# Optimization experiments

Measured on AMD Instinct MI355X. Metric: run time of the kernel, lower is better.

The kernel has to match this reference:

```python
import jax, jax.numpy as jnp
import numpy as np

N_NODES = 100000
N_EDGES = 1600000
IN_DIM = 256
OUT_DIM = 64
LEAKY_SLOPE = 0.01  # torch F.leaky_relu default


def setup_inputs() -> dict:
    key = jax.random.key(0)
    k1, k2, k3, k4, k5 = jax.random.split(key, 5)
    h = jax.random.normal(k1, (N_NODES, IN_DIM), dtype=jnp.float32)
    W_fc = jax.random.normal(k2, (IN_DIM, OUT_DIM), dtype=jnp.float32) * (1.0 / np.sqrt(IN_DIM))
    a_attn = jax.random.normal(k3, (2 * OUT_DIM,), dtype=jnp.float32) * (1.0 / np.sqrt(2 * OUT_DIM))
    edge_src = jax.random.randint(k4, (N_EDGES,), 0, N_NODES, dtype=jnp.int32)
    edge_dst = jax.random.randint(k5, (N_EDGES,), 0, N_NODES, dtype=jnp.int32)
    return {"h": h, "W_fc": W_fc, "a_attn": a_attn, "edge_src": edge_src, "edge_dst": edge_dst}


def reference(h, W_fc, a_attn, edge_src, edge_dst):
    # z = fc(h)  (no bias)
    z = h @ W_fc                                   # [N, D]
    # edge attention: leaky_relu(concat(z_src, z_dst) @ a)
    # split a into src/dst halves -> node-level projections (same math, no concat)
    el = z @ a_attn[:OUT_DIM]                      # [N]
    er = z @ a_attn[OUT_DIM:]                      # [N]
    e = jax.nn.leaky_relu(el[edge_src] + er[edge_dst], negative_slope=LEAKY_SLOPE)  # [E]
    # segment softmax over destination-node mailboxes
    m = jax.ops.segment_max(e, edge_dst, num_segments=N_NODES)   # [N]
    ex = jnp.exp(e - m[edge_dst])                                # [E]
    s = jax.ops.segment_sum(ex, edge_dst, num_segments=N_NODES)  # [N]
    alpha = ex / s[edge_dst]                                     # [E]
    # weighted scatter-sum of neighbor features
    h_out = jax.ops.segment_sum(alpha[:, None] * z[edge_src], edge_dst, num_segments=N_NODES)  # [N, D]
    # heads != 1 branch: ELU (dropout = 0 in eval)
    return jax.nn.elu(h_out)
```

## Files before the change

### kernel.cpp

```cpp
#include <hip/hip_runtime.h>
#include <hip/hip_bf16.h>

#define IN_DIM 256
#define OUT_DIM 64
#define CHUNK 4096
#define BSH 8
#define P2CAP 6144

typedef short bf16x8 __attribute__((ext_vector_type(8)));
typedef float f32x4 __attribute__((ext_vector_type(4)));

__device__ inline unsigned short f2bf(float x) {
  unsigned int u = __float_as_uint(x);
  return (unsigned short)((u + 0x7FFFu + ((u >> 16) & 1u)) >> 16);
}

__global__ __launch_bounds__(256) void k_prep(const float* __restrict__ W,
                                              unsigned short* __restrict__ Wbf) {
  int f = blockIdx.x * 256 + threadIdx.x;
  int kc = f >> 8, ct = (f >> 6) & 3, q = (f >> 4) & 3, nq = f & 15;
  int col = ct * 16 + nq, k0 = kc * 32 + q * 8;
  unsigned short v[8];
#pragma unroll
  for (int j = 0; j < 8; ++j) v[j] = f2bf(W[(size_t)(k0 + j) * OUT_DIM + col]);
  *(uint4*)(Wbf + (size_t)f * 8) = *(uint4*)v;
}

__global__ __launch_bounds__(256) void k_gemm(const float* __restrict__ h,
                                              const unsigned short* __restrict__ Wbf,
                                              const float* __restrict__ a,
                                              unsigned short* __restrict__ zb,
                                              float* __restrict__ el,
                                              float* __restrict__ er, int n) {
  __shared__ unsigned short Ab[64][264];
  const int t = threadIdx.x;
  const int base = blockIdx.x * 64;

#pragma unroll
  for (int i = 0; i < 16; ++i) {
    int f = i * 256 + t;
    int r = f >> 6, c4 = f & 63;
    int row = base + r;
    float4 v = make_float4(0.f, 0.f, 0.f, 0.f);
    if (row < n) v = *(const float4*)(h + (size_t)row * IN_DIM + c4 * 4);
    unsigned int p0 = (unsigned int)f2bf(v.x) | ((unsigned int)f2bf(v.y) << 16);
    unsigned int p1 = (unsigned int)f2bf(v.z) | ((unsigned int)f2bf(v.w) << 16);
    *(uint2*)&Ab[r][c4 * 4] = make_uint2(p0, p1);
  }
  __syncthreads();

  const int w = t >> 6, lane = t & 63, nq = lane & 15, q = lane >> 4;

  f32x4 acc[4];
#pragma unroll
  for (int ct = 0; ct < 4; ++ct) acc[ct] = (f32x4){0.f, 0.f, 0.f, 0.f};

#pragma unroll
  for (int kc = 0; kc < 8; ++kc) {
    bf16x8 af = *(const bf16x8*)&Ab[w * 16 + nq][kc * 32 + q * 8];
#pragma unroll
    for (int ct = 0; ct < 4; ++ct) {
      bf16x8 bfr = *(const bf16x8*)(Wbf + (size_t)((kc * 4 + ct) * 64 + lane) * 8);
      acc[ct] = __builtin_amdgcn_mfma_f32_16x16x32_bf16(af, bfr, acc[ct], 0, 0, 0);
    }
  }

  float a1[4], a2[4];
#pragma unroll
  for (int ct = 0; ct < 4; ++ct) {
    a1[ct] = a[ct * 16 + nq];
    a2[ct] = a[OUT_DIM + ct * 16 + nq];
  }
#pragma unroll
  for (int r = 0; r < 4; ++r) {
    int orow = base + w * 16 + q * 4 + r;
    float p1 = 0.f, p2 = 0.f;
#pragma unroll
    for (int ct = 0; ct < 4; ++ct) {
      float v = acc[ct][r];
      p1 += v * a1[ct];
      p2 += v * a2[ct];
      if (orow < n) zb[(size_t)orow * OUT_DIM + ct * 16 + nq] = f2bf(v);
    }
    p1 += __shfl_xor(p1, 1); p1 += __shfl_xor(p1, 2);
    p1 += __shfl_xor(p1, 4); p1 += __shfl_xor(p1, 8);
    p2 += __shfl_xor(p2, 1); p2 += __shfl_xor(p2, 2);
    p2 += __shfl_xor(p2, 4); p2 += __shfl_xor(p2, 8);
    if (orow < n && nq == 0) { el[orow] = p1; er[orow] = p2; }
  }
}

__global__ __launch_bounds__(256) void k_p1hist(const int* __restrict__ dst,
                                                int* __restrict__ gh, int E,
                                                int nbuck, int b1) {
  __shared__ int hist[512];
  int t = threadIdx.x, b = blockIdx.x;
  hist[t] = 0;
  hist[t + 256] = 0;
  __syncthreads();
  int beg = b * CHUNK;
#pragma unroll
  for (int i = t; i < CHUNK; i += 256) {
    int e = beg + i;
    if (e < E) atomicAdd(&hist[dst[e] >> BSH], 1);
  }
  __syncthreads();
  for (int i = t; i < nbuck; i += 256) gh[i * b1 + b] = hist[i];
}

__global__ __launch_bounds__(256) void k_scanA(const int* __restrict__ in,
                                               int* __restrict__ out,
                                               int* __restrict__ bsum, int N) {
  __shared__ int wtot[4];
  int t = threadIdx.x, lane = t & 63, w = t >> 6;
  int idx = blockIdx.x * 1024 + t * 4;
  int d0 = idx + 0 < N ? in[idx + 0] : 0;
  int d1 = idx + 1 < N ? in[idx + 1] : 0;
  int d2 = idx + 2 < N ? in[idx + 2] : 0;
  int d3 = idx + 3 < N ? in[idx + 3] : 0;
  int tsum = d0 + d1 + d2 + d3;
  int incl = tsum;
  for (int o = 1; o < 64; o <<= 1) {
    int v = __shfl_up(incl, o);
    if (lane >= o) incl += v;
  }
  if (lane == 63) wtot[w] = incl;
  __syncthreads();
  int woff = 0;
  for (int i = 0; i < 4; ++i)
    if (i < w) woff += wtot[i];
  int btot = wtot[0] + wtot[1] + wtot[2] + wtot[3];
  int e = woff + incl - tsum;
  if (idx + 0 < N) out[idx + 0] = e; e += d0;
  if (idx + 1 < N) out[idx + 1] = e; e += d1;
  if (idx + 2 < N) out[idx + 2] = e; e += d2;
  if (idx + 3 < N) out[idx + 3] = e;
  if (t == 0) bsum[blockIdx.x] = btot;
}

__global__ __launch_bounds__(256) void k_scanB(int* __restrict__ bsum, int nb) {
  __shared__ int wtot[4];
  int t = threadIdx.x, lane = t & 63, w = t >> 6;
  int v = t < nb ? bsum[t] : 0;
  int incl = v;
  for (int o = 1; o < 64; o <<= 1) {
    int u = __shfl_up(incl, o);
    if (lane >= o) incl += u;
  }
  if (lane == 63) wtot[w] = incl;
  __syncthreads();
  int woff = 0;
  for (int i = 0; i < 4; ++i)
    if (i < w) woff += wtot[i];
  if (t < nb) bsum[t] = woff + incl - v;
}

__global__ __launch_bounds__(256) void k_scanC2(int* __restrict__ out,
                                                const int* __restrict__ bsum, int M) {
  int i = blockIdx.x * 256 + threadIdx.x;
  if (i < M) out[i] += bsum[i >> 10];
}

__global__ __launch_bounds__(256) void k_p1scat(const int* __restrict__ src,
                                                const int* __restrict__ dst,
                                                const int* __restrict__ pbase,
                                                int2* __restrict__ pairs, int E,
                                                int nbuck, int b1) {
  __shared__ int pb[512];
  __shared__ int cur[512];
  int t = threadIdx.x, b = blockIdx.x;
  for (int i = t; i < 512; i += 256) {
    pb[i] = (i < nbuck) ? pbase[i * b1 + b] : 0;
    cur[i] = 0;
  }
  __syncthreads();
  int beg = b * CHUNK;
#pragma unroll
  for (int i = t; i < CHUNK; i += 256) {
    int e = beg + i;
    if (e < E) {
      int d = dst[e], s = src[e];
      int bk = d >> BSH;
      int r = atomicAdd(&cur[bk], 1);
      pairs[pb[bk] + r] = make_int2(d, s);
    }
  }
}

__global__ __launch_bounds__(256) void k_p2(const int2* __restrict__ pairs,
                                            const int* __restrict__ pbase,
                                            int* __restrict__ ssrc,
                                            int* __restrict__ off, int E, int n,
                                            int nbuck, int b1) {
  __shared__ int deg[256];
  __shared__ int loff[256];
  __shared__ int cur[256];
  __shared__ int stage[P2CAP];
  __shared__ int wtot[4];
  int t = threadIdx.x, b = blockIdx.x;
  int beg = pbase[b * b1];
  int end = (b + 1 < nbuck) ? pbase[(b + 1) * b1] : E;
  int cnt = end - beg;
  int base = b << BSH;
  deg[t] = 0;
  __syncthreads();
  for (int i = t; i < cnt; i += 256) atomicAdd(&deg[pairs[beg + i].x - base], 1);
  __syncthreads();
  int v = deg[t];
  int lane = t & 63, w = t >> 6;
  int inc = v;
  for (int o = 1; o < 64; o <<= 1) {
    int u = __shfl_up(inc, o);
    if (lane >= o) inc += u;
  }
  if (lane == 63) wtot[w] = inc;
  __syncthreads();
  int woff = 0;
  for (int i = 0; i < 4; ++i)
    if (i < w) woff += wtot[i];
  int ex = woff + inc - v;
  loff[t] = ex;
  cur[t] = ex;
  __syncthreads();
  for (int i = t; i < cnt; i += 256) {
    int2 p = pairs[beg + i];
    int r = atomicAdd(&cur[p.x - base], 1);
    if (r < P2CAP) stage[r] = p.y;
  }
  __syncthreads();
  for (int i = t; i < cnt; i += 256) ssrc[beg + i] = stage[i];
  int node = base + t;
  if (node <= n) off[node] = beg + loff[t];
}

__global__ __launch_bounds__(256) void k_agg(const int* __restrict__ off,
                                             const int* __restrict__ ssrc,
                                             const float* __restrict__ el,
                                             const float* __restrict__ er,
                                             const unsigned short* __restrict__ zb,
                                             float* __restrict__ out, int N) {
  int t = threadIdx.x;
  int node = blockIdx.x * 16 + (t >> 4);
  if (node >= N) return;
  int cq = (t & 15) * 4;
  int beg = off[node], end = off[node + 1];
  float erd = er[node];
  float ax = 0.f, ay = 0.f, az = 0.f, aw = 0.f, ssum = 0.f;
  int j = beg;
  for (; j + 4 <= end; j += 4) {
    int s0 = ssrc[j], s1 = ssrc[j + 1], s2 = ssrc[j + 2], s3 = ssrc[j + 3];
    uint2 z0 = *(const uint2*)(zb + (s0 << 6) + cq);
    uint2 z1 = *(const uint2*)(zb + (s1 << 6) + cq);
    uint2 z2 = *(const uint2*)(zb + (s2 << 6) + cq);
    uint2 z3 = *(const uint2*)(zb + (s3 << 6) + cq);
    float x0 = el[s0] + erd, x1 = el[s1] + erd;
    float x2 = el[s2] + erd, x3 = el[s3] + erd;
    x0 = x0 > 0.f ? x0 : 0.01f * x0;
    x1 = x1 > 0.f ? x1 : 0.01f * x1;
    x2 = x2 > 0.f ? x2 : 0.01f * x2;
    x3 = x3 > 0.f ? x3 : 0.01f * x3;
    float e0 = __expf(x0), e1 = __expf(x1), e2 = __expf(x2), e3 = __expf(x3);
    ssum += (e0 + e1) + (e2 + e3);
    ax += e0 * __uint_as_float(z0.x << 16) + e1 * __uint_as_float(z1.x << 16) +
          e2 * __uint_as_float(z2.x << 16) + e3 * __uint_as_float(z3.x << 16);
    ay += e0 * __uint_as_float(z0.x & 0xFFFF0000u) + e1 * __uint_as_float(z1.x & 0xFFFF0000u) +
          e2 * __uint_as_float(z2.x & 0xFFFF0000u) + e3 * __uint_as_float(z3.x & 0xFFFF0000u);
    az += e0 * __uint_as_float(z0.y << 16) + e1 * __uint_as_float(z1.y << 16) +
          e2 * __uint_as_float(z2.y << 16) + e3 * __uint_as_float(z3.y << 16);
    aw += e0 * __uint_as_float(z0.y & 0xFFFF0000u) + e1 * __uint_as_float(z1.y & 0xFFFF0000u) +
          e2 * __uint_as_float(z2.y & 0xFFFF0000u) + e3 * __uint_as_float(z3.y & 0xFFFF0000u);
  }
  for (; j < end; ++j) {
    int s = ssrc[j];
    uint2 zv = *(const uint2*)(zb + (s << 6) + cq);
    float x = el[s] + erd;
    x = x > 0.f ? x : 0.01f * x;
    float ex = __expf(x);
    ssum += ex;
    ax += ex * __uint_as_float(zv.x << 16);
    ay += ex * __uint_as_float(zv.x & 0xFFFF0000u);
    az += ex * __uint_as_float(zv.y << 16);
    aw += ex * __uint_as_float(zv.y & 0xFFFF0000u);
  }
  float4 o = make_float4(0.f, 0.f, 0.f, 0.f);
  if (end > beg) {
    float inv = 1.f / ssum;
    ax *= inv; ay *= inv; az *= inv; aw *= inv;
    o.x = ax > 0.f ? ax : __expf(ax) - 1.f;
    o.y = ay > 0.f ? ay : __expf(ay) - 1.f;
    o.z = az > 0.f ? az : __expf(az) - 1.f;
    o.w = aw > 0.f ? aw : __expf(aw) - 1.f;
  }
  *(float4*)(out + ((size_t)node << 6) + cq) = o;
}

extern "C" void kernel_launch(void* const* d_in, const int* in_sizes, int n_in,
                              void* d_out, int out_size, void* d_ws, size_t ws_size,
                              hipStream_t stream) {
  const float* h = (const float*)d_in[0];
  const float* W = (const float*)d_in[1];
  const float* a = (const float*)d_in[2];
  const int* src = (const int*)d_in[3];
  const int* dst = (const int*)d_in[4];
  const int n = in_sizes[0] / IN_DIM;
  const int E = in_sizes[3];
  float* out = (float*)d_out;

  const int b1 = (E + CHUNK - 1) / CHUNK;
  const int nbuck = (n + (1 << BSH) - 1) >> BSH;
  const int M = nbuck * b1;
  const int NB = (M + 1023) / 1024;

  char* ws = (char*)d_ws;
  auto alloc = [&](size_t bytes) {
    char* p = ws;
    ws += (bytes + 15) & ~(size_t)15;
    return p;
  };
  unsigned short* Wbf = (unsigned short*)alloc(16384 * 2);
  unsigned short* zb = (unsigned short*)alloc((size_t)n * OUT_DIM * 2);
  float* el = (float*)alloc((size_t)n * 4);
  float* er = (float*)alloc((size_t)n * 4);
  int* gh = (int*)alloc((size_t)M * 4);
  int* pbase = (int*)alloc((size_t)M * 4);
  int* bsum = (int*)alloc(256 * 4);
  int* off = (int*)alloc((size_t)(n + 1) * 4);
  int2* pairs = (int2*)alloc((size_t)E * 8);
  int* ssrc = (int*)alloc((size_t)E * 4);

  k_prep<<<8, 256, 0, stream>>>(W, Wbf);
  k_gemm<<<(n + 63) / 64, 256, 0, stream>>>(h, Wbf, a, zb, el, er, n);
  k_p1hist<<<b1, 256, 0, stream>>>(dst, gh, E, nbuck, b1);
  k_scanA<<<NB, 256, 0, stream>>>(gh, pbase, bsum, M);
  k_scanB<<<1, 256, 0, stream>>>(bsum, NB);
  k_scanC2<<<(M + 255) / 256, 256, 0, stream>>>(pbase, bsum, M);
  k_p1scat<<<b1, 256, 0, stream>>>(src, dst, pbase, pairs, E, nbuck, b1);
  k_p2<<<nbuck, 256, 0, stream>>>(pairs, pbase, ssrc, off, E, n, nbuck, b1);
  k_agg<<<(n + 15) / 16, 256, 0, stream>>>(off, ssrc, el, er, zb, out, n);
}
```

Baseline: 275.0 us.

## Replace two-pass bucket sort CSR build with global atomic counting sort

Replaces the bucketed two-level counting sort (chunk histograms, pair scatter, per-bucket local sort) with a per-node degree histogram built by global atomics, fused into the GEMM kernel, followed by a scan and a direct atomic scatter of source ids into CSR order. This removes the intermediate pairs buffer and two kernels, cutting memory traffic and launches. The cost is heavy global atomic contention and scattered writes, and the order of edges within each node's list becomes nondeterministic, which can change floating-point summation order in aggregation.

```diff
diff --git a/kernel.cpp b/kernel.cpp
--- a/kernel.cpp
+++ b/kernel.cpp
@@ -3,9 +3,6 @@
 
 #define IN_DIM 256
 #define OUT_DIM 64
-#define CHUNK 4096
-#define BSH 8
-#define P2CAP 6144
 
 typedef short bf16x8 __attribute__((ext_vector_type(8)));
 typedef float f32x4 __attribute__((ext_vector_type(4)));
@@ -31,7 +28,9 @@
                                               const float* __restrict__ a,
                                               unsigned short* __restrict__ zb,
                                               float* __restrict__ el,
-                                              float* __restrict__ er, int n) {
+                                              float* __restrict__ er, int n,
+                                              const int* __restrict__ dst,
+                                              int* __restrict__ cur, int E) {
   __shared__ unsigned short Ab[64][264];
   const int t = threadIdx.x;
   const int base = blockIdx.x * 64;
@@ -88,24 +87,21 @@
     p2 += __shfl_xor(p2, 4); p2 += __shfl_xor(p2, 8);
     if (orow < n && nq == 0) { el[orow] = p1; er[orow] = p2; }
   }
-}
-
-__global__ __launch_bounds__(256) void k_p1hist(const int* __restrict__ dst,
-                                                int* __restrict__ gh, int E,
-                                                int nbuck, int b1) {
-  __shared__ int hist[512];
-  int t = threadIdx.x, b = blockIdx.x;
-  hist[t] = 0;
-  hist[t + 256] = 0;
-  __syncthreads();
-  int beg = b * CHUNK;
-#pragma unroll
-  for (int i = t; i < CHUNK; i += 256) {
-    int e = beg + i;
-    if (e < E) atomicAdd(&hist[dst[e] >> BSH], 1);
-  }
-  __syncthreads();
-  for (int i = t; i < nbuck; i += 256) gh[i * b1 + b] = hist[i];
+
+  int e0 = blockIdx.x * 1024 + t * 4;
+  if (e0 + 4 <= E) {
+    int4 d4 = *(const int4*)(dst + e0);
+    atomicAdd(&cur[d4.x], 1);
+    atomicAdd(&cur[d4.y], 1);
+    atomicAdd(&cur[d4.z], 1);
+    atomicAdd(&cur[d4.w], 1);
+  } else {
+#pragma unroll
+    for (int k = 0; k < 4; ++k) {
+      int e = e0 + k;
+      if (e < E) atomicAdd(&cur[dst[e]], 1);
+    }
+  }
 }
 
 __global__ __launch_bounds__(256) void k_scanA(const int* __restrict__ in,
@@ -156,81 +152,35 @@
 }
 
 __global__ __launch_bounds__(256) void k_scanC2(int* __restrict__ out,
-                                                const int* __restrict__ bsum, int M) {
+                                                const int* __restrict__ bsum,
+                                                int* __restrict__ cur, int M) {
   int i = blockIdx.x * 256 + threadIdx.x;
-  if (i < M) out[i] += bsum[i >> 10];
-}
-
-__global__ __launch_bounds__(256) void k_p1scat(const int* __restrict__ src,
-                                                const int* __restrict__ dst,
-                                                const int* __restrict__ pbase,
-                                                int2* __restrict__ pairs, int E,
-                                                int nbuck, int b1) {
-  __shared__ int pb[512];
-  __shared__ int cur[512];
-  int t = threadIdx.x, b = blockIdx.x;
-  for (int i = t; i < 512; i += 256) {
-    pb[i] = (i < nbuck) ? pbase[i * b1 + b] : 0;
-    cur[i] = 0;
-  }
-  __syncthreads();
-  int beg = b * CHUNK;
-#pragma unroll
-  for (int i = t; i < CHUNK; i += 256) {
-    int e = beg + i;
-    if (e < E) {
-      int d = dst[e], s = src[e];
-      int bk = d >> BSH;
-      int r = atomicAdd(&cur[bk], 1);
-      pairs[pb[bk] + r] = make_int2(d, s);
-    }
-  }
-}
-
-__global__ __launch_bounds__(256) void k_p2(const int2* __restrict__ pairs,
-                                            const int* __restrict__ pbase,
-                                            int* __restrict__ ssrc,
-                                            int* __restrict__ off, int E, int n,
-                                            int nbuck, int b1) {
-  __shared__ int deg[256];
-  __shared__ int loff[256];
-  __shared__ int cur[256];
-  __shared__ int stage[P2CAP];
-  __shared__ int wtot[4];
-  int t = threadIdx.x, b = blockIdx.x;
-  int beg = pbase[b * b1];
-  int end = (b + 1 < nbuck) ? pbase[(b + 1) * b1] : E;
-  int cnt = end - beg;
-  int base = b << BSH;
-  deg[t] = 0;
-  __syncthreads();
-  for (int i = t; i < cnt; i += 256) atomicAdd(&deg[pairs[beg + i].x - base], 1);
-  __syncthreads();
-  int v = deg[t];
-  int lane = t & 63, w = t >> 6;
-  int inc = v;
-  for (int o = 1; o < 64; o <<= 1) {
-    int u = __shfl_up(inc, o);
-    if (lane >= o) inc += u;
-  }
-  if (lane == 63) wtot[w] = inc;
-  __syncthreads();
-  int woff = 0;
-  for (int i = 0; i < 4; ++i)
-    if (i < w) woff += wtot[i];
-  int ex = woff + inc - v;
-  loff[t] = ex;
-  cur[t] = ex;
-  __syncthreads();
-  for (int i = t; i < cnt; i += 256) {
-    int2 p = pairs[beg + i];
-    int r = atomicAdd(&cur[p.x - base], 1);
-    if (r < P2CAP) stage[r] = p.y;
-  }
-  __syncthreads();
-  for (int i = t; i < cnt; i += 256) ssrc[beg + i] = stage[i];
-  int node = base + t;
-  if (node <= n) off[node] = beg + loff[t];
+  if (i < M) {
+    int v = out[i] + bsum[i >> 10];
+    out[i] = v;
+    cur[i] = v;
+  }
+}
+
+__global__ __launch_bounds__(256) void k_scat(const int* __restrict__ src,
+                                              const int* __restrict__ dst,
+                                              int* __restrict__ cur,
+                                              int* __restrict__ ssrc, int E) {
+  int e0 = (blockIdx.x * 256 + threadIdx.x) * 4;
+  if (e0 + 4 <= E) {
+    int4 s4 = *(const int4*)(src + e0);
+    int4 d4 = *(const int4*)(dst + e0);
+    ssrc[atomicAdd(&cur[d4.x], 1)] = s4.x;
+    ssrc[atomicAdd(&cur[d4.y], 1)] = s4.y;
+    ssrc[atomicAdd(&cur[d4.z], 1)] = s4.z;
+    ssrc[atomicAdd(&cur[d4.w], 1)] = s4.w;
+  } else {
+#pragma unroll
+    for (int k = 0; k < 4; ++k) {
+      int e = e0 + k;
+      if (e < E) ssrc[atomicAdd(&cur[dst[e]], 1)] = src[e];
+    }
+  }
 }
 
 __global__ __launch_bounds__(256) void k_agg(const int* __restrict__ off,
@@ -306,11 +256,6 @@
   const int E = in_sizes[3];
   float* out = (float*)d_out;
 
-  const int b1 = (E + CHUNK - 1) / CHUNK;
-  const int nbuck = (n + (1 << BSH) - 1) >> BSH;
-  const int M = nbuck * b1;
-  const int NB = (M + 1023) / 1024;
-
   char* ws = (char*)d_ws;
   auto alloc = [&](size_t bytes) {
     char* p = ws;
@@ -321,20 +266,23 @@
   unsigned short* zb = (unsigned short*)alloc((size_t)n * OUT_DIM * 2);
   float* el = (float*)alloc((size_t)n * 4);
   float* er = (float*)alloc((size_t)n * 4);
-  int* gh = (int*)alloc((size_t)M * 4);
-  int* pbase = (int*)alloc((size_t)M * 4);
+  int* off = (int*)alloc((size_t)(n + 1) * 4);
+  int* cur = (int*)alloc((size_t)(n + 1) * 4);
   int* bsum = (int*)alloc(256 * 4);
-  int* off = (int*)alloc((size_t)(n + 1) * 4);
-  int2* pairs = (int2*)alloc((size_t)E * 8);
   int* ssrc = (int*)alloc((size_t)E * 4);
 
+  const int M = n + 1;
+  const int NB = (M + 1023) / 1024;
+  const int gemm_blocks = (n + 63) / 64;
+  const int edge_blocks = (E + 1023) / 1024;
+  const int gb = gemm_blocks > edge_blocks ? gemm_blocks : edge_blocks;
+
+  hipMemsetAsync(cur, 0, (size_t)M * 4, stream);
   k_prep<<<8, 256, 0, stream>>>(W, Wbf);
-  k_gemm<<<(n + 63) / 64, 256, 0, stream>>>(h, Wbf, a, zb, el, er, n);
-  k_p1hist<<<b1, 256, 0, stream>>>(dst, gh, E, nbuck, b1);
-  k_scanA<<<NB, 256, 0, stream>>>(gh, pbase, bsum, M);
+  k_gemm<<<gb, 256, 0, stream>>>(h, Wbf, a, zb, el, er, n, dst, cur, E);
+  k_scanA<<<NB, 256, 0, stream>>>(cur, off, bsum, M);
   k_scanB<<<1, 256, 0, stream>>>(bsum, NB);
-  k_scanC2<<<(M + 255) / 256, 256, 0, stream>>>(pbase, bsum, M);
-  k_p1scat<<<b1, 256, 0, stream>>>(src, dst, pbase, pairs, E, nbuck, b1);
-  k_p2<<<nbuck, 256, 0, stream>>>(pairs, pbase, ssrc, off, E, n, nbuck, b1);
+  k_scanC2<<<(M + 255) / 256, 256, 0, stream>>>(off, bsum, cur, M);
+  k_scat<<<edge_blocks, 256, 0, stream>>>(src, dst, cur, ssrc, E);
   k_agg<<<(n + 15) / 16, 256, 0, stream>>>(off, ssrc, el, er, zb, out, n);
 }
```

Result: slower. 404.5 us (+47.1%).

## Fuse histogram into GEMM, fold scan fixup into consumers, pack edge pairs

Applied to the files above, without the earlier changes.

The destination-bucket histogram now runs inside the GEMM kernel on its first b1 blocks, and the separate k_p1hist launch is removed. The k_scanC2 add-back pass is dropped: k_p1scat and k_p2 add the block sum to the partial scan value when they read it. Edge pairs are packed into one 32-bit int, with the local destination in the top 8 bits and the source in the low 24, which halves pairs traffic. This saves two launches and some memory bandwidth, but adds tail work to some GEMM blocks and assumes source ids fit in 24 bits.

```diff
diff --git a/kernel.cpp b/kernel.cpp
--- a/kernel.cpp
+++ b/kernel.cpp
@@ -31,8 +31,12 @@
                                               const float* __restrict__ a,
                                               unsigned short* __restrict__ zb,
                                               float* __restrict__ el,
-                                              float* __restrict__ er, int n) {
+                                              float* __restrict__ er, int n,
+                                              const int* __restrict__ dst,
+                                              int* __restrict__ gh, int E,
+                                              int nbuck, int b1) {
   __shared__ unsigned short Ab[64][264];
+  __shared__ int hist[512];
   const int t = threadIdx.x;
   const int base = blockIdx.x * 64;
 
@@ -88,24 +92,20 @@
     p2 += __shfl_xor(p2, 4); p2 += __shfl_xor(p2, 8);
     if (orow < n && nq == 0) { el[orow] = p1; er[orow] = p2; }
   }
-}
-
-__global__ __launch_bounds__(256) void k_p1hist(const int* __restrict__ dst,
-                                                int* __restrict__ gh, int E,
-                                                int nbuck, int b1) {
-  __shared__ int hist[512];
-  int t = threadIdx.x, b = blockIdx.x;
-  hist[t] = 0;
-  hist[t + 256] = 0;
-  __syncthreads();
-  int beg = b * CHUNK;
-#pragma unroll
-  for (int i = t; i < CHUNK; i += 256) {
-    int e = beg + i;
-    if (e < E) atomicAdd(&hist[dst[e] >> BSH], 1);
-  }
-  __syncthreads();
-  for (int i = t; i < nbuck; i += 256) gh[i * b1 + b] = hist[i];
+
+  if (blockIdx.x < b1) {
+    hist[t] = 0;
+    hist[t + 256] = 0;
+    __syncthreads();
+    int beg = blockIdx.x * CHUNK;
+#pragma unroll
+    for (int i = t; i < CHUNK; i += 256) {
+      int e = beg + i;
+      if (e < E) atomicAdd(&hist[dst[e] >> BSH], 1);
+    }
+    __syncthreads();
+    for (int i = t; i < nbuck; i += 256) gh[i * b1 + blockIdx.x] = hist[i];
+  }
 }
 
 __global__ __launch_bounds__(256) void k_scanA(const int* __restrict__ in,
@@ -155,22 +155,22 @@
   if (t < nb) bsum[t] = woff + incl - v;
 }
 
-__global__ __launch_bounds__(256) void k_scanC2(int* __restrict__ out,
-                                                const int* __restrict__ bsum, int M) {
-  int i = blockIdx.x * 256 + threadIdx.x;
-  if (i < M) out[i] += bsum[i >> 10];
-}
-
 __global__ __launch_bounds__(256) void k_p1scat(const int* __restrict__ src,
                                                 const int* __restrict__ dst,
                                                 const int* __restrict__ pbase,
-                                                int2* __restrict__ pairs, int E,
+                                                const int* __restrict__ bsum,
+                                                int* __restrict__ pairs, int E,
                                                 int nbuck, int b1) {
   __shared__ int pb[512];
   __shared__ int cur[512];
   int t = threadIdx.x, b = blockIdx.x;
   for (int i = t; i < 512; i += 256) {
-    pb[i] = (i < nbuck) ? pbase[i * b1 + b] : 0;
+    if (i < nbuck) {
+      int idx = i * b1 + b;
+      pb[i] = pbase[idx] + bsum[idx >> 10];
+    } else {
+      pb[i] = 0;
+    }
     cur[i] = 0;
   }
   __syncthreads();
@@ -182,13 +182,14 @@
       int d = dst[e], s = src[e];
       int bk = d >> BSH;
       int r = atomicAdd(&cur[bk], 1);
-      pairs[pb[bk] + r] = make_int2(d, s);
-    }
-  }
-}
-
-__global__ __launch_bounds__(256) void k_p2(const int2* __restrict__ pairs,
+      pairs[pb[bk] + r] = ((d & ((1 << BSH) - 1)) << 24) | s;
+    }
+  }
+}
+
+__global__ __launch_bounds__(256) void k_p2(const int* __restrict__ pairs,
                                             const int* __restrict__ pbase,
+                                            const int* __restrict__ bsum,
                                             int* __restrict__ ssrc,
                                             int* __restrict__ off, int E, int n,
                                             int nbuck, int b1) {
@@ -198,13 +199,20 @@
   __shared__ int stage[P2CAP];
   __shared__ int wtot[4];
   int t = threadIdx.x, b = blockIdx.x;
-  int beg = pbase[b * b1];
-  int end = (b + 1 < nbuck) ? pbase[(b + 1) * b1] : E;
+  int i0 = b * b1;
+  int beg = pbase[i0] + bsum[i0 >> 10];
+  int end;
+  if (b + 1 < nbuck) {
+    int i1 = (b + 1) * b1;
+    end = pbase[i1] + bsum[i1 >> 10];
+  } else {
+    end = E;
+  }
   int cnt = end - beg;
-  int base = b << BSH;
   deg[t] = 0;
   __syncthreads();
-  for (int i = t; i < cnt; i += 256) atomicAdd(&deg[pairs[beg + i].x - base], 1);
+  for (int i = t; i < cnt; i += 256)
+    atomicAdd(&deg[((unsigned)pairs[beg + i]) >> 24], 1);
   __syncthreads();
   int v = deg[t];
   int lane = t & 63, w = t >> 6;
@@ -223,13 +231,13 @@
   cur[t] = ex;
   __syncthreads();
   for (int i = t; i < cnt; i += 256) {
-    int2 p = pairs[beg + i];
-    int r = atomicAdd(&cur[p.x - base], 1);
-    if (r < P2CAP) stage[r] = p.y;
+    int p = pairs[beg + i];
+    int r = atomicAdd(&cur[((unsigned)p) >> 24], 1);
+    if (r < P2CAP) stage[r] = p & 0xFFFFFF;
   }
   __syncthreads();
   for (int i = t; i < cnt; i += 256) ssrc[beg + i] = stage[i];
-  int node = base + t;
+  int node = (b << BSH) + t;
   if (node <= n) off[node] = beg + loff[t];
 }
 
@@ -325,16 +333,14 @@
   int* pbase = (int*)alloc((size_t)M * 4);
   int* bsum = (int*)alloc(256 * 4);
   int* off = (int*)alloc((size_t)(n + 1) * 4);
-  int2* pairs = (int2*)alloc((size_t)E * 8);
+  int* pairs = (int*)alloc((size_t)E * 4);
   int* ssrc = (int*)alloc((size_t)E * 4);
 
   k_prep<<<8, 256, 0, stream>>>(W, Wbf);
-  k_gemm<<<(n + 63) / 64, 256, 0, stream>>>(h, Wbf, a, zb, el, er, n);
-  k_p1hist<<<b1, 256, 0, stream>>>(dst, gh, E, nbuck, b1);
+  k_gemm<<<(n + 63) / 64, 256, 0, stream>>>(h, Wbf, a, zb, el, er, n, dst, gh, E, nbuck, b1);
   k_scanA<<<NB, 256, 0, stream>>>(gh, pbase, bsum, M);
   k_scanB<<<1, 256, 0, stream>>>(bsum, NB);
-  k_scanC2<<<(M + 255) / 256, 256, 0, stream>>>(pbase, bsum, M);
-  k_p1scat<<<b1, 256, 0, stream>>>(src, dst, pbase, pairs, E, nbuck, b1);
-  k_p2<<<nbuck, 256, 0, stream>>>(pairs, pbase, ssrc, off, E, n, nbuck, b1);
+  k_p1scat<<<b1, 256, 0, stream>>>(src, dst, pbase, bsum, pairs, E, nbuck, b1);
+  k_p2<<<nbuck, 256, 0, stream>>>(pairs, pbase, bsum, ssrc, off, E, n, nbuck, b1);
   k_agg<<<(n + 15) / 16, 256, 0, stream>>>(off, ssrc, el, er, zb, out, n);
 }
```

Result: faster. 261.3 us (-5.0%).

## Fuse CSR partition passes into per-chunk local sort with packed pairs

Applied to the files above, without the earlier changes.

Replaces the histogram, three-kernel global scan and scatter with a single partition kernel. Each chunk sorts its edges by bucket locally in shared memory and writes packed (local dst, src) words along with per-chunk bucket offsets. The second pass then gathers its bucket's segments from every chunk. This removes several launches and halves the pair traffic by packing each pair into one 32-bit word, at the cost of segmented, less coalesced reads in k_p2 and a source-index limit of 24 bits.

```diff
diff --git a/kernel.cpp b/kernel.cpp
--- a/kernel.cpp
+++ b/kernel.cpp
@@ -16,8 +16,10 @@
 }
 
 __global__ __launch_bounds__(256) void k_prep(const float* __restrict__ W,
-                                              unsigned short* __restrict__ Wbf) {
+                                              unsigned short* __restrict__ Wbf,
+                                              int* __restrict__ tot) {
   int f = blockIdx.x * 256 + threadIdx.x;
+  if (f < 512) tot[f] = 0;
   int kc = f >> 8, ct = (f >> 6) & 3, q = (f >> 4) & 3, nq = f & 15;
   int col = ct * 16 + nq, k0 = kc * 32 + q * 8;
   unsigned short v[8];
@@ -90,146 +92,173 @@
   }
 }
 
-__global__ __launch_bounds__(256) void k_p1hist(const int* __restrict__ dst,
-                                                int* __restrict__ gh, int E,
-                                                int nbuck, int b1) {
+__global__ __launch_bounds__(256) void k_part(const int* __restrict__ src,
+                                              const int* __restrict__ dst,
+                                              int* __restrict__ pairs,
+                                              int* __restrict__ lofs,
+                                              int* __restrict__ tot, int E,
+                                              int nbuck, int b1) {
   __shared__ int hist[512];
-  int t = threadIdx.x, b = blockIdx.x;
+  __shared__ int excl[512];
+  __shared__ int cur[512];
+  __shared__ int stage[CHUNK];
+  __shared__ int wtot[4];
+  const int t = threadIdx.x, b = blockIdx.x;
+  const int beg = b * CHUNK;
+  const int cnt = min(CHUNK, E - beg);
+
   hist[t] = 0;
   hist[t + 256] = 0;
   __syncthreads();
-  int beg = b * CHUNK;
-#pragma unroll
-  for (int i = t; i < CHUNK; i += 256) {
-    int e = beg + i;
-    if (e < E) atomicAdd(&hist[dst[e] >> BSH], 1);
-  }
-  __syncthreads();
-  for (int i = t; i < nbuck; i += 256) gh[i * b1 + b] = hist[i];
-}
-
-__global__ __launch_bounds__(256) void k_scanA(const int* __restrict__ in,
-                                               int* __restrict__ out,
-                                               int* __restrict__ bsum, int N) {
+
+  int dv[16], sv[16];
+#pragma unroll
+  for (int k = 0; k < 16; ++k) {
+    int i = k * 256 + t;
+    dv[k] = -1;
+    if (i < cnt) {
+      dv[k] = dst[beg + i];
+      sv[k] = src[beg + i];
+      atomicAdd(&hist[dv[k] >> BSH], 1);
+    }
+  }
+  __syncthreads();
+
+  {
+    int d0 = hist[2 * t], d1 = hist[2 * t + 1];
+    int tsum = d0 + d1;
+    int lane = t & 63, w = t >> 6;
+    int incl = tsum;
+    for (int o = 1; o < 64; o <<= 1) {
+      int u = __shfl_up(incl, o);
+      if (lane >= o) incl += u;
+    }
+    if (lane == 63) wtot[w] = incl;
+    __syncthreads();
+    int woff = 0;
+    for (int i = 0; i < 4; ++i)
+      if (i < w) woff += wtot[i];
+    int ex = woff + incl - tsum;
+    excl[2 * t] = ex;
+    excl[2 * t + 1] = ex + d0;
+    cur[2 * t] = ex;
+    cur[2 * t + 1] = ex + d0;
+  }
+  __syncthreads();
+
+#pragma unroll
+  for (int k = 0; k < 16; ++k) {
+    if (dv[k] >= 0) {
+      int bk = dv[k] >> BSH;
+      int r = atomicAdd(&cur[bk], 1);
+      stage[r] = ((dv[k] & ((1 << BSH) - 1)) << 24) | sv[k];
+    }
+  }
+  __syncthreads();
+#pragma unroll
+  for (int k = 0; k < 16; ++k) {
+    int i = k * 256 + t;
+    if (i < cnt) pairs[beg + i] = stage[i];
+  }
+  for (int i = t; i <= nbuck; i += 256) lofs[(size_t)b * (nbuck + 1) + i] = excl[i];
+  for (int i = t; i < nbuck; i += 256)
+    if (hist[i]) atomicAdd(&tot[i], hist[i]);
+}
+
+__global__ __launch_bounds__(256) void k_scanT(const int* __restrict__ tot,
+                                               int* __restrict__ pbeg, int nbuck) {
   __shared__ int wtot[4];
-  int t = threadIdx.x, lane = t & 63, w = t >> 6;
-  int idx = blockIdx.x * 1024 + t * 4;
-  int d0 = idx + 0 < N ? in[idx + 0] : 0;
-  int d1 = idx + 1 < N ? in[idx + 1] : 0;
-  int d2 = idx + 2 < N ? in[idx + 2] : 0;
-  int d3 = idx + 3 < N ? in[idx + 3] : 0;
-  int tsum = d0 + d1 + d2 + d3;
+  int t = threadIdx.x;
+  int d0 = (2 * t < nbuck) ? tot[2 * t] : 0;
+  int d1 = (2 * t + 1 < nbuck) ? tot[2 * t + 1] : 0;
+  int tsum = d0 + d1;
+  int lane = t & 63, w = t >> 6;
   int incl = tsum;
   for (int o = 1; o < 64; o <<= 1) {
-    int v = __shfl_up(incl, o);
-    if (lane >= o) incl += v;
+    int u = __shfl_up(incl, o);
+    if (lane >= o) incl += u;
   }
   if (lane == 63) wtot[w] = incl;
   __syncthreads();
   int woff = 0;
   for (int i = 0; i < 4; ++i)
     if (i < w) woff += wtot[i];
-  int btot = wtot[0] + wtot[1] + wtot[2] + wtot[3];
-  int e = woff + incl - tsum;
-  if (idx + 0 < N) out[idx + 0] = e; e += d0;
-  if (idx + 1 < N) out[idx + 1] = e; e += d1;
-  if (idx + 2 < N) out[idx + 2] = e; e += d2;
-  if (idx + 3 < N) out[idx + 3] = e;
-  if (t == 0) bsum[blockIdx.x] = btot;
-}
-
-__global__ __launch_bounds__(256) void k_scanB(int* __restrict__ bsum, int nb) {
-  __shared__ int wtot[4];
-  int t = threadIdx.x, lane = t & 63, w = t >> 6;
-  int v = t < nb ? bsum[t] : 0;
-  int incl = v;
-  for (int o = 1; o < 64; o <<= 1) {
-    int u = __shfl_up(incl, o);
-    if (lane >= o) incl += u;
-  }
-  if (lane == 63) wtot[w] = incl;
-  __syncthreads();
-  int woff = 0;
-  for (int i = 0; i < 4; ++i)
-    if (i < w) woff += wtot[i];
-  if (t < nb) bsum[t] = woff + incl - v;
-}
-
-__global__ __launch_bounds__(256) void k_scanC2(int* __restrict__ out,
-                                                const int* __restrict__ bsum, int M) {
-  int i = blockIdx.x * 256 + threadIdx.x;
-  if (i < M) out[i] += bsum[i >> 10];
-}
-
-__global__ __launch_bounds__(256) void k_p1scat(const int* __restrict__ src,
-                                                const int* __restrict__ dst,
-                                                const int* __restrict__ pbase,
-                                                int2* __restrict__ pairs, int E,
-                                                int nbuck, int b1) {
-  __shared__ int pb[512];
-  __shared__ int cur[512];
-  int t = threadIdx.x, b = blockIdx.x;
-  for (int i = t; i < 512; i += 256) {
-    pb[i] = (i < nbuck) ? pbase[i * b1 + b] : 0;
-    cur[i] = 0;
-  }
-  __syncthreads();
-  int beg = b * CHUNK;
-#pragma unroll
-  for (int i = t; i < CHUNK; i += 256) {
-    int e = beg + i;
-    if (e < E) {
-      int d = dst[e], s = src[e];
-      int bk = d >> BSH;
-      int r = atomicAdd(&cur[bk], 1);
-      pairs[pb[bk] + r] = make_int2(d, s);
-    }
-  }
-}
-
-__global__ __launch_bounds__(256) void k_p2(const int2* __restrict__ pairs,
-                                            const int* __restrict__ pbase,
+  int ex = woff + incl - tsum;
+  pbeg[2 * t] = ex;
+  pbeg[2 * t + 1] = ex + d0;
+}
+
+__global__ __launch_bounds__(256) void k_p2(const int* __restrict__ pairs,
+                                            const int* __restrict__ lofs,
+                                            const int* __restrict__ tot,
+                                            const int* __restrict__ pbeg,
                                             int* __restrict__ ssrc,
                                             int* __restrict__ off, int E, int n,
                                             int nbuck, int b1) {
+  __shared__ int seg0[512];
+  __shared__ int slen[512];
   __shared__ int deg[256];
   __shared__ int loff[256];
   __shared__ int cur[256];
   __shared__ int stage[P2CAP];
   __shared__ int wtot[4];
-  int t = threadIdx.x, b = blockIdx.x;
-  int beg = pbase[b * b1];
-  int end = (b + 1 < nbuck) ? pbase[(b + 1) * b1] : E;
-  int cnt = end - beg;
-  int base = b << BSH;
+  const int t = threadIdx.x, b = blockIdx.x;
+  const int beg = pbeg[b];
+  const int cntb = tot[b];
+
+  for (int c = t; c < b1; c += 256) {
+    int s0 = lofs[(size_t)c * (nbuck + 1) + b];
+    int s1 = lofs[(size_t)c * (nbuck + 1) + b + 1];
+    seg0[c] = c * CHUNK + s0;
+    slen[c] = s1 - s0;
+  }
   deg[t] = 0;
   __syncthreads();
-  for (int i = t; i < cnt; i += 256) atomicAdd(&deg[pairs[beg + i].x - base], 1);
-  __syncthreads();
-  int v = deg[t];
-  int lane = t & 63, w = t >> 6;
-  int inc = v;
-  for (int o = 1; o < 64; o <<= 1) {
-    int u = __shfl_up(inc, o);
-    if (lane >= o) inc += u;
-  }
-  if (lane == 63) wtot[w] = inc;
-  __syncthreads();
-  int woff = 0;
-  for (int i = 0; i < 4; ++i)
-    if (i < w) woff += wtot[i];
-  int ex = woff + inc - v;
-  loff[t] = ex;
-  cur[t] = ex;
-  __syncthreads();
-  for (int i = t; i < cnt; i += 256) {
-    int2 p = pairs[beg + i];
-    int r = atomicAdd(&cur[p.x - base], 1);
-    if (r < P2CAP) stage[r] = p.y;
-  }
-  __syncthreads();
-  for (int i = t; i < cnt; i += 256) ssrc[beg + i] = stage[i];
-  int node = base + t;
+
+  const int w = t >> 6, li = t & 63;
+  for (int c = w; c < b1; c += 4) {
+    int s0 = seg0[c], ln = slen[c];
+    for (int k0 = 0; k0 < ln; k0 += 64) {
+      if (li < ln - k0) {
+        int v = pairs[s0 + k0 + li];
+        atomicAdd(&deg[((unsigned)v) >> 24], 1);
+      }
+    }
+  }
+  __syncthreads();
+
+  {
+    int v = deg[t];
+    int inc = v;
+    for (int o = 1; o < 64; o <<= 1) {
+      int u = __shfl_up(inc, o);
+      if (li >= o) inc += u;
+    }
+    if (li == 63) wtot[w] = inc;
+    __syncthreads();
+    int woff = 0;
+    for (int i = 0; i < 4; ++i)
+      if (i < w) woff += wtot[i];
+    int ex = woff + inc - v;
+    loff[t] = ex;
+    cur[t] = ex;
+  }
+  __syncthreads();
+
+  for (int c = w; c < b1; c += 4) {
+    int s0 = seg0[c], ln = slen[c];
+    for (int k0 = 0; k0 < ln; k0 += 64) {
+      if (li < ln - k0) {
+        int v = pairs[s0 + k0 + li];
+        int r = atomicAdd(&cur[((unsigned)v) >> 24], 1);
+        if (r < P2CAP) stage[r] = v & 0xFFFFFF;
+      }
+    }
+  }
+  __syncthreads();
+
+  for (int i = t; i < cntb; i += 256) ssrc[beg + i] = stage[i];
+  int node = (b << BSH) + t;
   if (node <= n) off[node] = beg + loff[t];
 }
 
@@ -308,8 +337,6 @@
 
   const int b1 = (E + CHUNK - 1) / CHUNK;
   const int nbuck = (n + (1 << BSH) - 1) >> BSH;
-  const int M = nbuck * b1;
-  const int NB = (M + 1023) / 1024;
 
   char* ws = (char*)d_ws;
   auto alloc = [&](size_t bytes) {
@@ -321,20 +348,17 @@
   unsigned short* zb = (unsigned short*)alloc((size_t)n * OUT_DIM * 2);
   float* el = (float*)alloc((size_t)n * 4);
   float* er = (float*)alloc((size_t)n * 4);
-  int* gh = (int*)alloc((size_t)M * 4);
-  int* pbase = (int*)alloc((size_t)M * 4);
-  int* bsum = (int*)alloc(256 * 4);
+  int* lofs = (int*)alloc((size_t)b1 * (nbuck + 1) * 4);
+  int* tot = (int*)alloc(512 * 4);
+  int* pbeg = (int*)alloc(512 * 4);
   int* off = (int*)alloc((size_t)(n + 1) * 4);
-  int2* pairs = (int2*)alloc((size_t)E * 8);
+  int* pairs = (int*)alloc((size_t)b1 * CHUNK * 4);
   int* ssrc = (int*)alloc((size_t)E * 4);
 
-  k_prep<<<8, 256, 0, stream>>>(W, Wbf);
+  k_prep<<<8, 256, 0, stream>>>(W, Wbf, tot);
   k_gemm<<<(n + 63) / 64, 256, 0, stream>>>(h, Wbf, a, zb, el, er, n);
-  k_p1hist<<<b1, 256, 0, stream>>>(dst, gh, E, nbuck, b1);
-  k_scanA<<<NB, 256, 0, stream>>>(gh, pbase, bsum, M);
-  k_scanB<<<1, 256, 0, stream>>>(bsum, NB);
-  k_scanC2<<<(M + 255) / 256, 256, 0, stream>>>(pbase, bsum, M);
-  k_p1scat<<<b1, 256, 0, stream>>>(src, dst, pbase, pairs, E, nbuck, b1);
-  k_p2<<<nbuck, 256, 0, stream>>>(pairs, pbase, ssrc, off, E, n, nbuck, b1);
+  k_part<<<b1, 256, 0, stream>>>(src, dst, pairs, lofs, tot, E, nbuck, b1);
+  k_scanT<<<1, 256, 0, stream>>>(tot, pbeg, nbuck);
+  k_p2<<<nbuck, 256, 0, stream>>>(pairs, lofs, tot, pbeg, ssrc, off, E, n, nbuck, b1);
   k_agg<<<(n + 15) / 16, 256, 0, stream>>>(off, ssrc, el, er, zb, out, n);
 }
```

Result: slower. 335.9 us (+22.1%).
